# Kernel tuning notes

Measured on AMD Instinct MI355X. Metric: run time of the kernel, lower is better.

The kernel has to match this reference:

```python
import jax, jax.numpy as jnp
import numpy as np

B, S, D = 4, 2048, 1024
H = 16
HD = D // H  # 64


def setup_inputs() -> dict:
    key = jax.random.key(0)
    ks = jax.random.split(key, 5)
    std = 1.0 / np.sqrt(D)
    return {
        "x": jax.random.normal(ks[0], (B, S, D), dtype=jnp.float32),
        "Wq": jax.random.normal(ks[1], (D, D), dtype=jnp.float32) * std,
        "Wk": jax.random.normal(ks[2], (D, D), dtype=jnp.float32) * std,
        "Wv": jax.random.normal(ks[3], (D, D), dtype=jnp.float32) * std,
        "Wo": jax.random.normal(ks[4], (D, D), dtype=jnp.float32) * std,
        "bo": jnp.zeros((D,), dtype=jnp.float32),
    }


def reference(x, Wq, Wk, Wv, Wo, bo):
    b, n, d_in = x.shape
    q = (x @ Wq).reshape(b, n, H, HD).transpose(0, 2, 1, 3)  # [b,h,n,hd]
    k = (x @ Wk).reshape(b, n, H, HD).transpose(0, 2, 1, 3)
    v = (x @ Wv).reshape(b, n, H, HD).transpose(0, 2, 1, 3)
    scores = jnp.einsum("bhqd,bhkd->bhqk", q, k)  # full NxN, as in original
    causal = jnp.tril(jnp.ones((n, n), dtype=bool))  # True = keep
    scores = jnp.where(causal, scores, -jnp.inf)
    attn = jax.nn.softmax(scores / np.sqrt(HD), axis=-1)
    # dropout p=0.0 -> identity
    ctx = jnp.einsum("bhqk,bhkd->bqhd", attn, v).reshape(b, n, H * HD)
    return ctx @ Wo + bo
```

## Files before the change

### kernel.cpp

```cpp
#include <hip/hip_runtime.h>
#include <math.h>

#define BATCH 4
#define SLEN 2048
#define DMODEL 1024
#define NH 16
#define HD 64
#define MROWS (BATCH * SLEN)
#define QK_LD 2048

typedef __attribute__((ext_vector_type(8))) short short8;
typedef __attribute__((ext_vector_type(4))) float floatx4;

#define AS1 __attribute__((address_space(1)))
#define AS3 __attribute__((address_space(3)))

__device__ inline unsigned short f2bf(float f) {
    union { float f; unsigned u; } a; a.f = f;
    unsigned r = a.u + 0x7fff + ((a.u >> 16) & 1);
    return (unsigned short)(r >> 16);
}

__device__ inline unsigned pack_bf(float lo, float hi) {
    union { float f; unsigned u; } a, b; a.f = lo; b.f = hi;
    return __builtin_amdgcn_perm(b.u + 0x8000u, a.u + 0x8000u, 0x07060302u);
}
__device__ inline unsigned pack_tr(float lo, float hi) {
    union { float f; unsigned u; } a, b; a.f = lo; b.f = hi;
    return __builtin_amdgcn_perm(b.u, a.u, 0x07060302u);
}


__global__ __launch_bounds__(256) void cvt_bf16(const float* __restrict__ src,
                                                short* __restrict__ dst) {
    int i = (blockIdx.x * 256 + threadIdx.x) * 4;
    float4 v = *(const float4*)(src + i);
    unsigned short t0 = f2bf(v.x), t1 = f2bf(v.y), t2 = f2bf(v.z), t3 = f2bf(v.w);
    uint2 o;
    o.x = (unsigned)t0 | ((unsigned)t1 << 16);
    o.y = (unsigned)t2 | ((unsigned)t3 << 16);
    *(uint2*)(dst + i) = o;
}

__global__ __launch_bounds__(256) void cvt_wT4(
    const float* __restrict__ Wq, const float* __restrict__ Wk,
    const float* __restrict__ Wv, const float* __restrict__ Wo,
    short* __restrict__ WqkT, short* __restrict__ WvT, short* __restrict__ WoT)
{
    const float* W; short* Wt; float sc = 1.0f;
    int z = blockIdx.z;
    if (z == 0)      { W = Wq; Wt = WqkT; sc = 0.18033688011112042f; }
    else if (z == 1) { W = Wk; Wt = WqkT + (size_t)DMODEL * DMODEL; }
    else if (z == 2) { W = Wv; Wt = WvT; }
    else             { W = Wo; Wt = WoT; }

    __shared__ float t[32][33];
    int bn = blockIdx.x * 32, bk = blockIdx.y * 32;
    int tx = threadIdx.x & 31, r0 = (threadIdx.x >> 5) * 4;
    #pragma unroll
    for (int i = 0; i < 4; i++)
        t[r0 + i][tx] = W[(size_t)(bk + r0 + i) * DMODEL + bn + tx];
    __syncthreads();
    #pragma unroll
    for (int i = 0; i < 4; i++)
        Wt[(size_t)(bn + r0 + i) * DMODEL + bk + tx] = (short)f2bf(t[tx][r0 + i] * sc);
}

#define TM 128
#define TN 128
#define TK 32

template <int OUT_BF16>
__global__ __launch_bounds__(256) void mfma_gemm(
    const short* __restrict__ A,
    const short* __restrict__ Bt,
    const float* __restrict__ bias,
    void* __restrict__ Cout, int M, int N, int K)
{
    __shared__ short As[TM * TK];
    __shared__ short Bs[TN * TK];
    int tid = threadIdx.x;
    int m0 = blockIdx.y * TM, n0 = blockIdx.x * TN;
    int l = tid & 63, w = tid >> 6;
    int wm = (w >> 1) * 64, wn = (w & 1) * 64;
    int lr = l & 15, lk = (l >> 4) * 8;

    floatx4 acc[4][4] = {};

    for (int k0 = 0; k0 < K; k0 += TK) {
        #pragma unroll
        for (int r = 0; r < 2; r++) {
            int c = r * 256 + tid;
            int mm = c >> 2, kk = (c & 3) * 8;
            __builtin_amdgcn_global_load_lds(
                (const AS1 void*)(A + (size_t)(m0 + mm) * K + k0 + kk),
                (AS3 void*)(As + c * 8), 16, 0, 0);
            __builtin_amdgcn_global_load_lds(
                (const AS1 void*)(Bt + (size_t)(n0 + mm) * K + k0 + kk),
                (AS3 void*)(Bs + c * 8), 16, 0, 0);
        }
        __syncthreads();

        short8 af[4], bg[4];
        #pragma unroll
        for (int i = 0; i < 4; i++) {
            af[i] = *(const short8*)(As + (wm + i * 16 + lr) * TK + lk);
            bg[i] = *(const short8*)(Bs + (wn + i * 16 + lr) * TK + lk);
        }
        #pragma unroll
        for (int mi = 0; mi < 4; mi++)
            #pragma unroll
            for (int ni = 0; ni < 4; ni++)
                acc[mi][ni] = __builtin_amdgcn_mfma_f32_16x16x32_bf16(
                    af[mi], bg[ni], acc[mi][ni], 0, 0, 0);
        __syncthreads();
    }

    int rbase = (l >> 4) * 4, cbase = l & 15;
    if (OUT_BF16) {
        short* C = (short*)Cout;
        #pragma unroll
        for (int mi = 0; mi < 4; mi++)
            #pragma unroll
            for (int r = 0; r < 4; r++) {
                int row = m0 + wm + mi * 16 + rbase + r;
                #pragma unroll
                for (int ni = 0; ni < 4; ni++) {
                    int col = n0 + wn + ni * 16 + cbase;
                    C[(size_t)row * N + col] = (short)f2bf(acc[mi][ni][r]);
                }
            }
    } else {
        float* C = (float*)Cout;
        #pragma unroll
        for (int mi = 0; mi < 4; mi++)
            #pragma unroll
            for (int r = 0; r < 4; r++) {
                int row = m0 + wm + mi * 16 + rbase + r;
                #pragma unroll
                for (int ni = 0; ni < 4; ni++) {
                    int col = n0 + wn + ni * 16 + cbase;
                    C[(size_t)row * N + col] = acc[mi][ni][r] + bias[col];
                }
            }
    }
}

#define PSTR 72

__global__ __launch_bounds__(256) void fa_mfma(
    const short* __restrict__ QK, const short* __restrict__ VtT,
    short* __restrict__ ctx)
{
    __shared__ __align__(16) short Ks[2][64][32];
    __shared__ __align__(16) short Vs[2][64][32];
    __shared__ __align__(16) short Ps[4][16][PSTR];

    int tid = threadIdx.x;
    int l = tid & 63, w = tid >> 6;
    int lr = l & 15, lg = l >> 4;
    int bh = blockIdx.x;
    int b = bh >> 4, h = bh & 15;
    int p = blockIdx.y;

    const short* Qbase = QK + (size_t)b * SLEN * QK_LD + h * HD;
    const short* Kbase = Qbase + 1024;
    const short* Vbase = VtT + (size_t)h * HD * MROWS + b * SLEN;

    int xoff = (lg ^ ((lr >> 1) & 3)) * 8;

    short8 ones;
    #pragma unroll
    for (int j = 0; j < 8; j++) ones[j] = (short)0x3F80;

    #pragma unroll 1
    for (int half = 0; half < 2; half++) {
        int qt = (half == 0) ? (31 - p) : p;
        int q0 = qt * 64;
        int qrow = q0 + w * 16 + lr;

        short8 qf[2];
        #pragma unroll
        for (int kk = 0; kk < 2; kk++)
            qf[kk] = *(const short8*)(Qbase + (size_t)qrow * QK_LD + kk * 32 + lg * 8);

        floatx4 O[4] = {};
        floatx4 accL = {};

        for (int kt = 0; kt <= qt; kt++) {
            int k0 = kt * 64;
            __syncthreads();
            #pragma unroll
            for (int r2 = 0; r2 < 2; r2++) {
                int c = r2 * 256 + tid;
                int kh = c >> 8, rr = (c >> 2) & 63;
                int q = (c & 3) ^ ((rr >> 1) & 3);
                __builtin_amdgcn_global_load_lds(
                    (const AS1 void*)(Kbase + (size_t)(k0 + rr) * QK_LD + kh * 32 + q * 8),
                    (AS3 void*)(&Ks[0][0][0] + c * 8), 16, 0, 0);
                __builtin_amdgcn_global_load_lds(
                    (const AS1 void*)(Vbase + (size_t)rr * MROWS + k0 + kh * 32 + q * 8),
                    (AS3 void*)(&Vs[0][0][0] + c * 8), 16, 0, 0);
            }
            __syncthreads();

            floatx4 s4[4] = {};
            #pragma unroll
            for (int kk = 0; kk < 2; kk++)
                #pragma unroll
                for (int t = 0; t < 4; t++) {
                    short8 kf = *(const short8*)(&Ks[kk][t * 16 + lr][xoff]);
                    s4[t] = __builtin_amdgcn_mfma_f32_16x16x32_bf16(kf, qf[kk], s4[t], 0, 0, 0);
                }

            if (kt == qt) {
                #pragma unroll
                for (int t = 0; t < 4; t++)
                    #pragma unroll
                    for (int r = 0; r < 4; r++)
                        if (k0 + t * 16 + lg * 4 + r > qrow) s4[t][r] = -INFINITY;
            }

            #pragma unroll
            for (int t = 0; t < 4; t++) {
                float p0 = exp2f(s4[t][0]);
                float p1 = exp2f(s4[t][1]);
                float p2 = exp2f(s4[t][2]);
                float p3 = exp2f(s4[t][3]);
                uint2 pk;
                pk.x = pack_tr(p0, p1);
                pk.y = pack_tr(p2, p3);
                *(uint2*)(&Ps[w][lr][t * 16 + lg * 4]) = pk;
            }

            #pragma unroll
            for (int kk = 0; kk < 2; kk++) {
                short8 pf = *(const short8*)(&Ps[w][lr][kk * 32 + lg * 8]);
                accL = __builtin_amdgcn_mfma_f32_16x16x32_bf16(ones, pf, accL, 0, 0, 0);
                #pragma unroll
                for (int dt = 0; dt < 4; dt++) {
                    short8 vf = *(const short8*)(&Vs[kk][dt * 16 + lr][xoff]);
                    O[dt] = __builtin_amdgcn_mfma_f32_16x16x32_bf16(vf, pf, O[dt], 0, 0, 0);
                }
            }
        }

        float linv = 1.f / accL[0];
        short* crow = ctx + ((size_t)b * SLEN + qrow) * DMODEL + h * HD;
        #pragma unroll
        for (int dt = 0; dt < 4; dt++) {
            uint2 pk;
            pk.x = pack_bf(O[dt][0] * linv, O[dt][1] * linv);
            pk.y = pack_bf(O[dt][2] * linv, O[dt][3] * linv);
            *(uint2*)(crow + dt * 16 + lg * 4) = pk;
        }
    }
}

extern "C" void kernel_launch(void* const* d_in, const int* in_sizes, int n_in,
                              void* d_out, int out_size, void* d_ws, size_t ws_size,
                              hipStream_t stream) {
    const float* x  = (const float*)d_in[0];
    const float* Wq = (const float*)d_in[1];
    const float* Wk = (const float*)d_in[2];
    const float* Wv = (const float*)d_in[3];
    const float* Wo = (const float*)d_in[4];
    const float* bo = (const float*)d_in[5];
    float* out = (float*)d_out;

    const size_t tsz = (size_t)MROWS * DMODEL;
    const size_t wsz = (size_t)DMODEL * DMODEL;

    short* xb    = (short*)d_ws;
    short* WqkT  = xb + tsz;
    short* WvT   = WqkT + 2 * wsz;
    short* WoT   = WvT + wsz;
    short* QKb   = WoT + wsz;
    short* VtT   = QKb + 2 * tsz;
    short* Cb    = VtT + tsz;

    cvt_bf16<<<(int)(tsz / (256 * 4)), 256, 0, stream>>>(x, xb);
    cvt_wT4<<<dim3(32, 32, 4), 256, 0, stream>>>(Wq, Wk, Wv, Wo, WqkT, WvT, WoT);

    mfma_gemm<1><<<dim3(2048 / TN, MROWS / TM), 256, 0, stream>>>(
        xb, WqkT, nullptr, QKb, MROWS, 2048, DMODEL);
    mfma_gemm<1><<<dim3(MROWS / TN, DMODEL / TM), 256, 0, stream>>>(
        WvT, xb, nullptr, VtT, DMODEL, MROWS, DMODEL);

    fa_mfma<<<dim3(BATCH * NH, 16), 256, 0, stream>>>(QKb, VtT, Cb);

    mfma_gemm<0><<<dim3(DMODEL / TN, MROWS / TM), 256, 0, stream>>>(
        Cb, WoT, bo, out, MROWS, DMODEL, DMODEL);
}
```

Measured before the change: 285.9 us.

## Process both paired query tiles in one pass sharing K/V tile loads

The attention kernel now processes the two paired query tiles (31-p and p) at the same time instead of one after the other. Each loaded K/V tile is used by both, with the short tile's work predicated off once it finishes, so K/V tiles for the short half are no longer loaded twice. The change also switches to the raw exp2 builtin and adds a min-blocks hint to the launch bounds. In exchange it doubles accumulator registers and P shared buffers, which may cause spills or lower occupancy.

```diff
diff --git a/kernel.cpp b/kernel.cpp
--- a/kernel.cpp
+++ b/kernel.cpp
@@ -148,13 +148,14 @@
 
 #define PSTR 72
 
-__global__ __launch_bounds__(256) void fa_mfma(
+__global__ __launch_bounds__(256, 4) void fa_mfma(
     const short* __restrict__ QK, const short* __restrict__ VtT,
     short* __restrict__ ctx)
 {
     __shared__ __align__(16) short Ks[2][64][32];
     __shared__ __align__(16) short Vs[2][64][32];
-    __shared__ __align__(16) short Ps[4][16][PSTR];
+    __shared__ __align__(16) short PsA[4][16][PSTR];
+    __shared__ __align__(16) short PsB[4][16][PSTR];
 
     int tid = threadIdx.x;
     int l = tid & 63, w = tid >> 6;
@@ -173,85 +174,126 @@
     #pragma unroll
     for (int j = 0; j < 8; j++) ones[j] = (short)0x3F80;
 
-    #pragma unroll 1
-    for (int half = 0; half < 2; half++) {
-        int qt = (half == 0) ? (31 - p) : p;
-        int q0 = qt * 64;
-        int qrow = q0 + w * 16 + lr;
-
-        short8 qf[2];
+    int qtA = 31 - p, qtB = p;
+    int qrowA = qtA * 64 + w * 16 + lr;
+    int qrowB = qtB * 64 + w * 16 + lr;
+
+    short8 qfA[2], qfB[2];
+    #pragma unroll
+    for (int kk = 0; kk < 2; kk++) {
+        qfA[kk] = *(const short8*)(Qbase + (size_t)qrowA * QK_LD + kk * 32 + lg * 8);
+        qfB[kk] = *(const short8*)(Qbase + (size_t)qrowB * QK_LD + kk * 32 + lg * 8);
+    }
+
+    floatx4 OA[4] = {}, OB[4] = {};
+    floatx4 accLA = {}, accLB = {};
+
+    for (int kt = 0; kt <= qtA; kt++) {
+        int k0 = kt * 64;
+        bool actB = (kt <= qtB);
+        __syncthreads();
+        #pragma unroll
+        for (int r2 = 0; r2 < 2; r2++) {
+            int c = r2 * 256 + tid;
+            int kh = c >> 8, rr = (c >> 2) & 63;
+            int q = (c & 3) ^ ((rr >> 1) & 3);
+            __builtin_amdgcn_global_load_lds(
+                (const AS1 void*)(Kbase + (size_t)(k0 + rr) * QK_LD + kh * 32 + q * 8),
+                (AS3 void*)(&Ks[0][0][0] + c * 8), 16, 0, 0);
+            __builtin_amdgcn_global_load_lds(
+                (const AS1 void*)(Vbase + (size_t)rr * MROWS + k0 + kh * 32 + q * 8),
+                (AS3 void*)(&Vs[0][0][0] + c * 8), 16, 0, 0);
+        }
+        __syncthreads();
+
+        floatx4 sA[4] = {}, sB[4] = {};
         #pragma unroll
         for (int kk = 0; kk < 2; kk++)
-            qf[kk] = *(const short8*)(Qbase + (size_t)qrow * QK_LD + kk * 32 + lg * 8);
-
-        floatx4 O[4] = {};
-        floatx4 accL = {};
-
-        for (int kt = 0; kt <= qt; kt++) {
-            int k0 = kt * 64;
-            __syncthreads();
-            #pragma unroll
-            for (int r2 = 0; r2 < 2; r2++) {
-                int c = r2 * 256 + tid;
-                int kh = c >> 8, rr = (c >> 2) & 63;
-                int q = (c & 3) ^ ((rr >> 1) & 3);
-                __builtin_amdgcn_global_load_lds(
-                    (const AS1 void*)(Kbase + (size_t)(k0 + rr) * QK_LD + kh * 32 + q * 8),
-                    (AS3 void*)(&Ks[0][0][0] + c * 8), 16, 0, 0);
-                __builtin_amdgcn_global_load_lds(
-                    (const AS1 void*)(Vbase + (size_t)rr * MROWS + k0 + kh * 32 + q * 8),
-                    (AS3 void*)(&Vs[0][0][0] + c * 8), 16, 0, 0);
-            }
-            __syncthreads();
-
-            floatx4 s4[4] = {};
-            #pragma unroll
-            for (int kk = 0; kk < 2; kk++)
+            #pragma unroll
+            for (int t = 0; t < 4; t++) {
+                short8 kf = *(const short8*)(&Ks[kk][t * 16 + lr][xoff]);
+                sA[t] = __builtin_amdgcn_mfma_f32_16x16x32_bf16(kf, qfA[kk], sA[t], 0, 0, 0);
+                if (actB)
+                    sB[t] = __builtin_amdgcn_mfma_f32_16x16x32_bf16(kf, qfB[kk], sB[t], 0, 0, 0);
+            }
+
+        if (kt == qtA) {
+            #pragma unroll
+            for (int t = 0; t < 4; t++)
                 #pragma unroll
-                for (int t = 0; t < 4; t++) {
-                    short8 kf = *(const short8*)(&Ks[kk][t * 16 + lr][xoff]);
-                    s4[t] = __builtin_amdgcn_mfma_f32_16x16x32_bf16(kf, qf[kk], s4[t], 0, 0, 0);
-                }
-
-            if (kt == qt) {
+                for (int r = 0; r < 4; r++)
+                    if (k0 + t * 16 + lg * 4 + r > qrowA) sA[t][r] = -INFINITY;
+        }
+        #pragma unroll
+        for (int t = 0; t < 4; t++) {
+            float p0 = __builtin_amdgcn_exp2f(sA[t][0]);
+            float p1 = __builtin_amdgcn_exp2f(sA[t][1]);
+            float p2 = __builtin_amdgcn_exp2f(sA[t][2]);
+            float p3 = __builtin_amdgcn_exp2f(sA[t][3]);
+            uint2 pk;
+            pk.x = pack_tr(p0, p1);
+            pk.y = pack_tr(p2, p3);
+            *(uint2*)(&PsA[w][lr][t * 16 + lg * 4]) = pk;
+        }
+        if (actB) {
+            if (kt == qtB) {
                 #pragma unroll
                 for (int t = 0; t < 4; t++)
                     #pragma unroll
                     for (int r = 0; r < 4; r++)
-                        if (k0 + t * 16 + lg * 4 + r > qrow) s4[t][r] = -INFINITY;
-            }
-
+                        if (k0 + t * 16 + lg * 4 + r > qrowB) sB[t][r] = -INFINITY;
+            }
             #pragma unroll
             for (int t = 0; t < 4; t++) {
-                float p0 = exp2f(s4[t][0]);
-                float p1 = exp2f(s4[t][1]);
-                float p2 = exp2f(s4[t][2]);
-                float p3 = exp2f(s4[t][3]);
+                float p0 = __builtin_amdgcn_exp2f(sB[t][0]);
+                float p1 = __builtin_amdgcn_exp2f(sB[t][1]);
+                float p2 = __builtin_amdgcn_exp2f(sB[t][2]);
+                float p3 = __builtin_amdgcn_exp2f(sB[t][3]);
                 uint2 pk;
                 pk.x = pack_tr(p0, p1);
                 pk.y = pack_tr(p2, p3);
-                *(uint2*)(&Ps[w][lr][t * 16 + lg * 4]) = pk;
-            }
-
-            #pragma unroll
-            for (int kk = 0; kk < 2; kk++) {
-                short8 pf = *(const short8*)(&Ps[w][lr][kk * 32 + lg * 8]);
-                accL = __builtin_amdgcn_mfma_f32_16x16x32_bf16(ones, pf, accL, 0, 0, 0);
-                #pragma unroll
-                for (int dt = 0; dt < 4; dt++) {
-                    short8 vf = *(const short8*)(&Vs[kk][dt * 16 + lr][xoff]);
-                    O[dt] = __builtin_amdgcn_mfma_f32_16x16x32_bf16(vf, pf, O[dt], 0, 0, 0);
-                }
-            }
-        }
-
-        float linv = 1.f / accL[0];
-        short* crow = ctx + ((size_t)b * SLEN + qrow) * DMODEL + h * HD;
+                *(uint2*)(&PsB[w][lr][t * 16 + lg * 4]) = pk;
+            }
+        }
+
+        #pragma unroll
+        for (int kk = 0; kk < 2; kk++) {
+            short8 pfA = *(const short8*)(&PsA[w][lr][kk * 32 + lg * 8]);
+            accLA = __builtin_amdgcn_mfma_f32_16x16x32_bf16(ones, pfA, accLA, 0, 0, 0);
+            short8 pfB;
+            if (actB) {
+                pfB = *(const short8*)(&PsB[w][lr][kk * 32 + lg * 8]);
+                accLB = __builtin_amdgcn_mfma_f32_16x16x32_bf16(ones, pfB, accLB, 0, 0, 0);
+            }
+            #pragma unroll
+            for (int dt = 0; dt < 4; dt++) {
+                short8 vf = *(const short8*)(&Vs[kk][dt * 16 + lr][xoff]);
+                OA[dt] = __builtin_amdgcn_mfma_f32_16x16x32_bf16(vf, pfA, OA[dt], 0, 0, 0);
+                if (actB)
+                    OB[dt] = __builtin_amdgcn_mfma_f32_16x16x32_bf16(vf, pfB, OB[dt], 0, 0, 0);
+            }
+        }
+    }
+
+    {
+        float linv = 1.f / accLA[0];
+        short* crow = ctx + ((size_t)b * SLEN + qrowA) * DMODEL + h * HD;
         #pragma unroll
         for (int dt = 0; dt < 4; dt++) {
             uint2 pk;
-            pk.x = pack_bf(O[dt][0] * linv, O[dt][1] * linv);
-            pk.y = pack_bf(O[dt][2] * linv, O[dt][3] * linv);
+            pk.x = pack_bf(OA[dt][0] * linv, OA[dt][1] * linv);
+            pk.y = pack_bf(OA[dt][2] * linv, OA[dt][3] * linv);
+            *(uint2*)(crow + dt * 16 + lg * 4) = pk;
+        }
+    }
+    {
+        float linv = 1.f / accLB[0];
+        short* crow = ctx + ((size_t)b * SLEN + qrowB) * DMODEL + h * HD;
+        #pragma unroll
+        for (int dt = 0; dt < 4; dt++) {
+            uint2 pk;
+            pk.x = pack_bf(OB[dt][0] * linv, OB[dt][1] * linv);
+            pk.y = pack_bf(OB[dt][2] * linv, OB[dt][3] * linv);
             *(uint2*)(crow + dt * 16 + lg * 4) = pk;
         }
     }
```

Result: slower. 415.2 us (+45.2%).
